# Optimization experiments

Measured on AMD Instinct MI355X. Metric: run time of the kernel, lower is better.

## Reference

```python
import jax, jax.numpy as jnp
import numpy as np

HIDDEN = 1024
D_INNER = 2048
DT_RANK = 64
STATE = 16
KCONV = 4


def setup_inputs() -> dict:
    key = jax.random.key(0)
    ks = jax.random.split(key, 9)
    s = lambda k, shape, sc=0.02: jax.random.normal(k, shape, dtype=jnp.float32) * sc
    return {
        "x": jax.random.normal(ks[0], (2, 1024, HIDDEN), dtype=jnp.float32),
        "in_proj_w": s(ks[1], (2 * D_INNER, HIDDEN)),
        "conv_w": s(ks[2], (D_INNER, 1, KCONV), 0.2),
        "conv_b": s(ks[3], (D_INNER,), 0.1),
        "x_proj_w": s(ks[4], (DT_RANK + 2 * STATE, D_INNER)),
        "dt_proj_w": s(ks[5], (D_INNER, DT_RANK), 0.1),
        "dt_proj_b": s(ks[6], (D_INNER,), 0.1),
        "A_log": s(ks[7], (D_INNER, STATE), 0.5),
        "out_proj_w": s(ks[8], (HIDDEN, D_INNER)),
    }


def _selective_scan(u, delta, A, B, C):
    # u, delta: (b,l,d); A: (d,n); B, C: (b,l,n)
    deltaA = jnp.exp(delta[..., None] * A)               # (b,l,d,n)
    dBu = (delta * u)[..., None] * B[:, :, None, :]      # (b,l,d,n)
    # scan over time axis; carry h: (b,d,n)
    deltaA_t = jnp.moveaxis(deltaA, 1, 0)                # (l,b,d,n)
    dBu_t = jnp.moveaxis(dBu, 1, 0)                      # (l,b,d,n)
    C_t = jnp.moveaxis(C, 1, 0)                          # (l,b,n)

    def step(h, inp):
        dA_i, dBu_i, C_i = inp
        h = dA_i * h + dBu_i
        y = jnp.einsum('bdn,bn->bd', h, C_i)
        return h, y

    h0 = jnp.zeros(u.shape[:1] + u.shape[2:] + (A.shape[1],), dtype=u.dtype)
    _, ys = jax.lax.scan(step, h0, (deltaA_t, dBu_t, C_t))
    return jnp.moveaxis(ys, 0, 1)                        # (b,l,d)


def reference(x, in_proj_w, conv_w, conv_b, x_proj_w, dt_proj_w, dt_proj_b, A_log, out_proj_w):
    b, l, _ = x.shape
    xr = x @ in_proj_w.T                                 # (b,l,2*d_inner)
    xs, res = jnp.split(xr, 2, axis=-1)
    # causal depthwise conv1d: pad left k-1 (matches padding=k-1 then [:l])
    xc = jnp.moveaxis(xs, 1, 2)                          # (b,d,l)
    xc = jax.lax.conv_general_dilated(
        xc, conv_w, window_strides=(1,), padding=[(KCONV - 1, 0)],
        feature_group_count=D_INNER,
        dimension_numbers=('NCH', 'OIH', 'NCH'))
    xc = xc + conv_b[None, :, None]
    xs = jnp.moveaxis(xc, 2, 1)                          # (b,l,d)
    xs = jax.nn.silu(xs)
    x_dbl = xs @ x_proj_w.T                              # (b,l,dt_rank+2n)
    dt, B, C = jnp.split(x_dbl, [DT_RANK, DT_RANK + STATE], axis=-1)
    delta = jax.nn.softplus(dt @ dt_proj_w.T + dt_proj_b)
    A = -jnp.exp(A_log.astype(jnp.float32))
    y = _selective_scan(xs, delta, A, B, C)
    y = y * jax.nn.silu(res)
    return y @ out_proj_w.T
```

## Files before the change

kernel.cpp:

```cpp
#include <hip/hip_runtime.h>

typedef unsigned short u16;
typedef __bf16 bf16x8 __attribute__((ext_vector_type(8)));
typedef float f32x4 __attribute__((ext_vector_type(4)));

__device__ inline float bf2f(u16 u) {
    unsigned int x = ((unsigned int)u) << 16;
    return __builtin_bit_cast(float, x);
}
__device__ inline u16 f2bf(float f) {
    unsigned int x = __builtin_bit_cast(unsigned int, f);
    return (u16)((x + 0x7FFFu + ((x >> 16) & 1u)) >> 16);
}
__device__ inline float sigm(float v) { return 1.f / (1.f + __expf(-v)); }
__device__ inline float ex2(float x) {
    float r; asm("v_exp_f32 %0, %1" : "=v"(r) : "v"(x)); return r;
}

__device__ __forceinline__ void gload16(const void* g, void* l) {
    __builtin_amdgcn_global_load_lds(
        (const __attribute__((address_space(1))) void*)g,
        (__attribute__((address_space(3))) void*)l, 16, 0, 0);
}

__device__ inline uint4 pack8(const float* p) {
    const float4* q = (const float4*)p;
    float4 a = q[0], b = q[1];
    union { u16 h[8]; uint4 v; } u;
    u.h[0] = f2bf(a.x); u.h[1] = f2bf(a.y); u.h[2] = f2bf(a.z); u.h[3] = f2bf(a.w);
    u.h[4] = f2bf(b.x); u.h[5] = f2bf(b.y); u.h[6] = f2bf(b.z); u.h[7] = f2bf(b.w);
    return u.v;
}

__global__ __launch_bounds__(256)
void cvt_front(const float* __restrict__ x, const float* __restrict__ inw,
               const float* __restrict__ xpw, const float* __restrict__ convw,
               const float* __restrict__ dtw,
               u16* __restrict__ x_bf, u16* __restrict__ inw_bf,
               u16* __restrict__ xpw_bf, float* __restrict__ wt,
               u16* __restrict__ dtw_bf)
{
    int bk = blockIdx.x, tid = threadIdx.x;
    if (bk < 1024) {
        int i = bk * 256 + tid;
        ((uint4*)x_bf)[i] = pack8(x + (size_t)i * 8);
    } else if (bk < 3072) {
        int i = (bk - 1024) * 256 + tid;
        ((uint4*)inw_bf)[i] = pack8(inw + (size_t)i * 8);
    } else if (bk < 3200) {
        int i = (bk - 3072) * 256 + tid;
        int row = (i * 8) >> 11;
        ((uint4*)xpw_bf)[i] = (row < 96) ? pack8(xpw + (size_t)row * 2048 + ((i * 8) & 2047))
                                         : make_uint4(0u, 0u, 0u, 0u);
    } else if (bk < 3264) {
        int i = (bk - 3200) * 256 + tid;
        ((uint4*)dtw_bf)[i] = pack8(dtw + (size_t)i * 8);
    } else {
        int i = (bk - 3264) * 256 + tid;
        wt[(i & 3) * 2048 + (i >> 2)] = convw[i];
    }
}

__global__ __launch_bounds__(256)
void cvt_bf16(const float* __restrict__ in, u16* __restrict__ out)
{
    int i = blockIdx.x * 256 + threadIdx.x;
    ((uint4*)out)[i] = pack8(in + (size_t)i * 8);
}

template<int EPI, bool OUTF32>
__global__ __launch_bounds__(256, 4)
void gemm2(const u16* __restrict__ A, int lda,
           const u16* __restrict__ B, int ldb,
           void* __restrict__ Cout, int ldc,
           int N, int ksplit, size_t zElems,
           const float* __restrict__ bias)
{
    __shared__ u16 sA[128][64];
    __shared__ u16 sB[128][64];

    const int tid  = threadIdx.x;
    const int lane = tid & 63;
    const int wave = tid >> 6;

    int nxy = gridDim.x * gridDim.y;
    int id  = blockIdx.y * gridDim.x + blockIdx.x;
    int bx, by;
    if ((nxy & 7) == 0) {
        int cpx = nxy >> 3;
        int swz = (id & 7) * cpx + (id >> 3);
        bx = swz % gridDim.x;
        by = swz / gridDim.x;
    } else { bx = blockIdx.x; by = blockIdx.y; }

    const int wm = (wave >> 1) * 64;
    const int wn = (wave & 1) * 64;
    const int m0 = by * 128;
    const int n0 = bx * 128;
    const int lm = lane & 15;
    const int g  = lane >> 4;
    const int k0 = blockIdx.z * ksplit;

    const int rr = lane >> 3;
    const int sl = lane & 7;
    const int xsl = sl ^ rr;
    const u16* gA = A + (size_t)(m0 + wave * 8 + rr) * lda + k0 + xsl * 8;
    const u16* gB = B + (size_t)(n0 + wave * 8 + rr) * ldb + k0 + xsl * 8;
    const int ldsRow = (wave * 8) * 128;

    f32x4 acc[4][4] = {};

    for (int kb = 0; kb < ksplit; kb += 64) {
        #pragma unroll
        for (int c = 0; c < 4; ++c) {
            gload16(gA + (size_t)c * 32 * lda + kb, (char*)sA + c * 4096 + ldsRow);
            gload16(gB + (size_t)c * 32 * ldb + kb, (char*)sB + c * 4096 + ldsRow);
        }
        __syncthreads();

        bf16x8 af[2][4], bfr[2][4];
        #pragma unroll
        for (int h = 0; h < 2; ++h) {
            #pragma unroll
            for (int i = 0; i < 4; ++i) {
                int ra = wm + i * 16 + lm;
                int rb = wn + i * 16 + lm;
                int chunk = (((h << 2) | g) ^ (lm & 7)) << 4;
                af[h][i]  = *(const bf16x8*)((const char*)sA + ra * 128 + chunk);
                bfr[h][i] = *(const bf16x8*)((const char*)sB + rb * 128 + chunk);
            }
        }
        #pragma unroll
        for (int h = 0; h < 2; ++h)
            #pragma unroll
            for (int i = 0; i < 4; ++i)
                #pragma unroll
                for (int j = 0; j < 4; ++j)
                    acc[i][j] = __builtin_amdgcn_mfma_f32_16x16x32_bf16(af[h][i], bfr[h][j], acc[i][j], 0, 0, 0);
        __syncthreads();
    }

    #pragma unroll
    for (int i = 0; i < 4; ++i) {
        int crow = m0 + wm + i * 16 + ((lane >> 4) << 2);
        #pragma unroll
        for (int j = 0; j < 4; ++j) {
            int ccol = n0 + wn + j * 16 + lm;
            if (ccol < N) {
                #pragma unroll
                for (int r = 0; r < 4; ++r) {
                    float v = acc[i][j][r];
                    if (EPI == 1) { v += bias[ccol]; v = (v > 20.f) ? v : log1pf(__expf(v)); }
                    if (EPI == 2 && ccol >= 2048) v *= sigm(v);
                    size_t off = (size_t)blockIdx.z * zElems + (size_t)(crow + r) * ldc + ccol;
                    if (OUTF32) ((float*)Cout)[off] = v;
                    else        ((u16*)Cout)[off]   = f2bf(v);
                }
            }
        }
    }
}

template<int EPI, bool OUTF32>
__global__ __launch_bounds__(256, 4)
void gemm_w(const u16* __restrict__ A, int lda,
            const u16* __restrict__ B, int ldb,
            void* __restrict__ Cout, int ldc,
            int N, int ksplit, size_t zElems,
            const float* __restrict__ bias)
{
    __shared__ u16 sA[64][64];
    __shared__ u16 sB[128][64];

    const int tid  = threadIdx.x;
    const int lane = tid & 63;
    const int wave = tid >> 6;

    int nxy = gridDim.x * gridDim.y;
    int id  = blockIdx.y * gridDim.x + blockIdx.x;
    int bx, by;
    if ((nxy & 7) == 0) {
        int cpx = nxy >> 3;
        int swz = (id & 7) * cpx + (id >> 3);
        bx = swz % gridDim.x;
        by = swz / gridDim.x;
    } else { bx = blockIdx.x; by = blockIdx.y; }

    const int wm = (wave >> 1) * 32;
    const int wn = (wave & 1) * 64;
    const int m0 = by * 64;
    const int n0 = bx * 128;
    const int lm = lane & 15;
    const int g  = lane >> 4;
    const int k0 = blockIdx.z * ksplit;

    const int rr = lane >> 3;
    const int sl = lane & 7;
    const int xsl = sl ^ rr;
    const u16* gA = A + (size_t)(m0 + wave * 8 + rr) * lda + k0 + xsl * 8;
    const u16* gB = B + (size_t)(n0 + wave * 8 + rr) * ldb + k0 + xsl * 8;
    const int ldsRow = (wave * 8) * 128;

    f32x4 acc[2][4] = {};

    for (int kb = 0; kb < ksplit; kb += 64) {
        #pragma unroll
        for (int c = 0; c < 2; ++c)
            gload16(gA + (size_t)c * 32 * lda + kb, (char*)sA + c * 4096 + ldsRow);
        #pragma unroll
        for (int c = 0; c < 4; ++c)
            gload16(gB + (size_t)c * 32 * ldb + kb, (char*)sB + c * 4096 + ldsRow);
        __syncthreads();

        bf16x8 af[2][2], bfr[2][4];
        #pragma unroll
        for (int h = 0; h < 2; ++h) {
            int chunk = (((h << 2) | g) ^ (lm & 7)) << 4;
            #pragma unroll
            for (int i = 0; i < 2; ++i)
                af[h][i]  = *(const bf16x8*)((const char*)sA + (wm + i * 16 + lm) * 128 + chunk);
            #pragma unroll
            for (int j = 0; j < 4; ++j)
                bfr[h][j] = *(const bf16x8*)((const char*)sB + (wn + j * 16 + lm) * 128 + chunk);
        }
        #pragma unroll
        for (int h = 0; h < 2; ++h)
            #pragma unroll
            for (int i = 0; i < 2; ++i)
                #pragma unroll
                for (int j = 0; j < 4; ++j)
                    acc[i][j] = __builtin_amdgcn_mfma_f32_16x16x32_bf16(af[h][i], bfr[h][j], acc[i][j], 0, 0, 0);
        __syncthreads();
    }

    #pragma unroll
    for (int i = 0; i < 2; ++i) {
        int crow = m0 + wm + i * 16 + ((lane >> 4) << 2);
        #pragma unroll
        for (int j = 0; j < 4; ++j) {
            int ccol = n0 + wn + j * 16 + lm;
            if (ccol < N) {
                #pragma unroll
                for (int r = 0; r < 4; ++r) {
                    float v = acc[i][j][r];
                    if (EPI == 1) { v += bias[ccol]; v = (v > 20.f) ? v : log1pf(__expf(v)); }
                    if (EPI == 2 && ccol >= 2048) v *= sigm(v);
                    size_t off = (size_t)blockIdx.z * zElems + (size_t)(crow + r) * ldc + ccol;
                    if (OUTF32) ((float*)Cout)[off] = v;
                    else        ((u16*)Cout)[off]   = f2bf(v);
                }
            }
        }
    }
}

template<int EPI, bool OUTF32>
__global__ __launch_bounds__(256, 4)
void gemm_s(const u16* __restrict__ A, int lda,
            const u16* __restrict__ B, int ldb,
            void* __restrict__ Cout, int ldc,
            int N, int ksplit, size_t zElems,
            const float* __restrict__ bias)
{
    __shared__ u16 sA[64][64];
    __shared__ u16 sB[64][64];

    const int tid  = threadIdx.x;
    const int lane = tid & 63;
    const int wave = tid >> 6;

    int nxy = gridDim.x * gridDim.y;
    int id  = blockIdx.y * gridDim.x + blockIdx.x;
    int bx, by;
    if ((nxy & 7) == 0) {
        int cpx = nxy >> 3;
        int swz = (id & 7) * cpx + (id >> 3);
        bx = swz % gridDim.x;
        by = swz / gridDim.x;
    } else { bx = blockIdx.x; by = blockIdx.y; }

    const int wm = (wave >> 1) * 32;
    const int wn = (wave & 1) * 32;
    const int m0 = by * 64;
    const int n0 = bx * 64;
    const int lm = lane & 15;
    const int g  = lane >> 4;
    const int k0 = blockIdx.z * ksplit;

    const int rr = lane >> 3;
    const int sl = lane & 7;
    const int xsl = sl ^ rr;
    const u16* gA = A + (size_t)(m0 + wave * 8 + rr) * lda + k0 + xsl * 8;
    const u16* gB = B + (size_t)(n0 + wave * 8 + rr) * ldb + k0 + xsl * 8;
    const int ldsRow = (wave * 8) * 128;

    f32x4 acc[2][2] = {};

    for (int kb = 0; kb < ksplit; kb += 64) {
        #pragma unroll
        for (int c = 0; c < 2; ++c) {
            gload16(gA + (size_t)c * 32 * lda + kb, (char*)sA + c * 4096 + ldsRow);
            gload16(gB + (size_t)c * 32 * ldb + kb, (char*)sB + c * 4096 + ldsRow);
        }
        __syncthreads();

        bf16x8 af[2][2], bfr[2][2];
        #pragma unroll
        for (int h = 0; h < 2; ++h) {
            #pragma unroll
            for (int i = 0; i < 2; ++i) {
                int ra = wm + i * 16 + lm;
                int rb = wn + i * 16 + lm;
                int chunk = (((h << 2) | g) ^ (lm & 7)) << 4;
                af[h][i]  = *(const bf16x8*)((const char*)sA + ra * 128 + chunk);
                bfr[h][i] = *(const bf16x8*)((const char*)sB + rb * 128 + chunk);
            }
        }
        #pragma unroll
        for (int h = 0; h < 2; ++h)
            #pragma unroll
            for (int i = 0; i < 2; ++i)
                #pragma unroll
                for (int j = 0; j < 2; ++j)
                    acc[i][j] = __builtin_amdgcn_mfma_f32_16x16x32_bf16(af[h][i], bfr[h][j], acc[i][j], 0, 0, 0);
        __syncthreads();
    }

    #pragma unroll
    for (int i = 0; i < 2; ++i) {
        int crow = m0 + wm + i * 16 + ((lane >> 4) << 2);
        #pragma unroll
        for (int j = 0; j < 2; ++j) {
            int ccol = n0 + wn + j * 16 + lm;
            if (ccol < N) {
                #pragma unroll
                for (int r = 0; r < 4; ++r) {
                    float v = acc[i][j][r];
                    if (EPI == 1) { v += bias[ccol]; v = (v > 20.f) ? v : log1pf(__expf(v)); }
                    size_t off = (size_t)blockIdx.z * zElems + (size_t)(crow + r) * ldc + ccol;
                    if (OUTF32) ((float*)Cout)[off] = v;
                    else        ((u16*)Cout)[off]   = f2bf(v);
                }
            }
        }
    }
}

__global__ __launch_bounds__(256)
void reduce96(const float* __restrict__ splits, u16* __restrict__ xdbl)
{
    int i = blockIdx.x * 256 + threadIdx.x;
    float acc = 0.f;
    #pragma unroll
    for (int z = 0; z < 8; ++z) acc += splits[(size_t)z * 196608 + i];
    xdbl[i] = f2bf(acc);
}

__global__ __launch_bounds__(256)
void reduce_out(const u16* __restrict__ parts, float* __restrict__ out)
{
    int i = blockIdx.x * 256 + threadIdx.x;
    float acc[8] = {};
    #pragma unroll
    for (int z = 0; z < 4; ++z) {
        uint4 v = ((const uint4*)(parts + (size_t)z * 2097152))[i];
        const u16* h = (const u16*)&v;
        #pragma unroll
        for (int e = 0; e < 8; ++e) acc[e] += bf2f(h[e]);
    }
    float4* o = (float4*)(out + (size_t)i * 8);
    o[0] = make_float4(acc[0], acc[1], acc[2], acc[3]);
    o[1] = make_float4(acc[4], acc[5], acc[6], acc[7]);
}

__global__ __launch_bounds__(256)
void conv_silu(const u16* __restrict__ xr, const float* __restrict__ wt,
               const float* __restrict__ bias, u16* __restrict__ xs)
{
    int gi = blockIdx.x * 256 + threadIdx.x;
    int d  = (gi & 255) * 8;
    int t0 = ((gi >> 8) & 255) * 4;
    int b  = gi >> 16;
    const u16* base = xr + (size_t)b * 4194304 + d;

    float bi[8], w8[4][8];
    {
        const float4* bp = (const float4*)(bias + d);
        float4 b0 = bp[0], b1 = bp[1];
        bi[0]=b0.x; bi[1]=b0.y; bi[2]=b0.z; bi[3]=b0.w;
        bi[4]=b1.x; bi[5]=b1.y; bi[6]=b1.z; bi[7]=b1.w;
        #pragma unroll
        for (int j = 0; j < 4; ++j) {
            const float4* wp = (const float4*)(wt + j * 2048 + d);
            float4 w0 = wp[0], w1 = wp[1];
            w8[j][0]=w0.x; w8[j][1]=w0.y; w8[j][2]=w0.z; w8[j][3]=w0.w;
            w8[j][4]=w1.x; w8[j][5]=w1.y; w8[j][6]=w1.z; w8[j][7]=w1.w;
        }
    }

    uint4 v[7];
    #pragma unroll
    for (int r = 0; r < 7; ++r) {
        int ti = t0 - 3 + r;
        v[r] = (ti >= 0) ? *(const uint4*)(base + (size_t)ti * 4096)
                         : make_uint4(0u, 0u, 0u, 0u);
    }

    #pragma unroll
    for (int tt = 0; tt < 4; ++tt) {
        float acc[8];
        #pragma unroll
        for (int e = 0; e < 8; ++e) acc[e] = bi[e];
        #pragma unroll
        for (int j = 0; j < 4; ++j) {
            const u16* h = (const u16*)&v[tt + j];
            #pragma unroll
            for (int e = 0; e < 8; ++e) acc[e] = fmaf(w8[j][e], bf2f(h[e]), acc[e]);
        }
        union { u16 h[8]; uint4 u; } o;
        #pragma unroll
        for (int e = 0; e < 8; ++e) { float x = acc[e]; o.h[e] = f2bf(x * sigm(x)); }
        *(uint4*)(xs + (size_t)b * 2097152 + (size_t)(t0 + tt) * 2048 + d) = o.u;
    }
}

template<int PHC>
__global__ __launch_bounds__(256)
void scan_chunk(const u16* __restrict__ deltag, u16* __restrict__ xsg,
                const u16* __restrict__ xdbl, const float* __restrict__ A_log,
                const u16* __restrict__ xr, float* __restrict__ summ,
                float* __restrict__ ssum)
{
    const int tid = threadIdx.x;
    const int d0 = blockIdx.x * 256;
    const int c  = blockIdx.y;
    const int b  = blockIdx.z;
    const int d  = d0 + tid;
    const int tok0 = b * 1024 + c * 32;

    __shared__ u16 s_del[32][256];
    __shared__ u16 s_uu[32][256];
    __shared__ u16 s_bc[32][32];
    __shared__ u16 s_res[PHC ? 32 : 1][PHC ? 256 : 1];
    __shared__ u16 s_y[PHC ? 32 : 1][PHC ? 256 : 1];

    for (int i = tid; i < 1024; i += 256) {
        int tl = i >> 5, v = i & 31;
        size_t tok = (size_t)(tok0 + tl);
        *(uint4*)&s_del[tl][v * 8] = *(const uint4*)&deltag[tok * 4096 + d0 + v * 8];
        *(uint4*)&s_uu[tl][v * 8]  = *(const uint4*)&xsg[tok * 2048 + d0 + v * 8];
        if (PHC)
            *(uint4*)&s_res[tl][v * 8] = *(const uint4*)&xr[tok * 4096 + 2048 + d0 + v * 8];
    }
    for (int i = tid; i < 1024; i += 256) {
        int tl = i >> 5, j = i & 31;
        s_bc[tl][j] = xdbl[(size_t)(tok0 + tl) * 96 + 64 + j];
    }

    float Ar[16], h[16];
    {
        const float4* Ap = (const float4*)(A_log + (size_t)d * 16);
        #pragma unroll
        for (int q = 0; q < 4; ++q) {
            float4 a = Ap[q];
            Ar[q * 4 + 0] = -__expf(a.x) * 1.44269504f;
            Ar[q * 4 + 1] = -__expf(a.y) * 1.44269504f;
            Ar[q * 4 + 2] = -__expf(a.z) * 1.44269504f;
            Ar[q * 4 + 3] = -__expf(a.w) * 1.44269504f;
        }
    }
    if (PHC) {
        const float4* hp = (const float4*)&summ[((size_t)(b * 32 + c) * 2048 + d) * 16];
        #pragma unroll
        for (int q = 0; q < 4; ++q) {
            float4 v = hp[q];
            h[q * 4 + 0] = v.x; h[q * 4 + 1] = v.y; h[q * 4 + 2] = v.z; h[q * 4 + 3] = v.w;
        }
    } else {
        #pragma unroll
        for (int n = 0; n < 16; ++n) h[n] = 0.f;
    }
    __syncthreads();

    float S = 0.f;
    #pragma unroll 4
    for (int tl = 0; tl < 32; ++tl) {
        float dlt = bf2f(s_del[tl][tid]);
        float du = dlt * bf2f(s_uu[tl][tid]);
        if (!PHC) S += dlt;
        #pragma unroll
        for (int n = 0; n < 16; ++n)
            h[n] = fmaf(ex2(dlt * Ar[n]), h[n], du * bf2f(s_bc[tl][n]));
        if (PHC) {
            float y = 0.f;
            #pragma unroll
            for (int n = 0; n < 16; ++n)
                y = fmaf(h[n], bf2f(s_bc[tl][16 + n]), y);
            s_y[tl][tid] = f2bf(y * bf2f(s_res[tl][tid]));
        }
    }

    if (!PHC) {
        float4* bp = (float4*)&summ[((size_t)(b * 32 + c) * 2048 + d) * 16];
        #pragma unroll
        for (int q = 0; q < 4; ++q)
            bp[q] = make_float4(h[q * 4], h[q * 4 + 1], h[q * 4 + 2], h[q * 4 + 3]);
        ssum[(size_t)(b * 32 + c) * 2048 + d] = S;
    } else {
        __syncthreads();
        for (int i = tid; i < 1024; i += 256) {
            int tl = i >> 5, v = i & 31;
            *(uint4*)&xsg[(size_t)(tok0 + tl) * 2048 + d0 + v * 8] = *(uint4*)&s_y[tl][v * 8];
        }
    }
}

__global__ __launch_bounds__(256)
void scan_phaseB(float* __restrict__ summ, const float* __restrict__ ssum,
                 const float* __restrict__ A_log)
{
    int g = blockIdx.x * 256 + threadIdx.x;
    int n = g & 15;
    int d = (g >> 4) & 2047;
    int b = g >> 15;
    float An2 = -__expf(A_log[(size_t)d * 16 + n]) * 1.44269504f;
    size_t base = ((size_t)(b * 32) * 2048 + d) * 16 + n;
    float bc[32], Sc[32];
    #pragma unroll
    for (int c = 0; c < 32; ++c) bc[c] = summ[base + (size_t)c * 32768];
    #pragma unroll
    for (int c = 0; c < 32; ++c) Sc[c] = ssum[(size_t)(b * 32 + c) * 2048 + d];
    float h = 0.f;
    #pragma unroll
    for (int c = 0; c < 32; ++c) {
        float nb = bc[c];
        bc[c] = h;
        h = fmaf(ex2(An2 * Sc[c]), h, nb);
    }
    #pragma unroll
    for (int c = 0; c < 32; ++c) summ[base + (size_t)c * 32768] = bc[c];
}

__global__ void sentinel_kernel(float* out, float v) { out[0] = v; }

extern "C" void kernel_launch(void* const* d_in, const int* in_sizes, int n_in,
                              void* d_out, int out_size, void* d_ws, size_t ws_size,
                              hipStream_t stream)
{
    const float* x         = (const float*)d_in[0];
    const float* in_w      = (const float*)d_in[1];
    const float* conv_w    = (const float*)d_in[2];
    const float* conv_b    = (const float*)d_in[3];
    const float* xproj_w   = (const float*)d_in[4];
    const float* dtproj_w  = (const float*)d_in[5];
    const float* dtproj_b  = (const float*)d_in[6];
    const float* A_log     = (const float*)d_in[7];
    const float* outproj_w = (const float*)d_in[8];
    float* out = (float*)d_out;

    static const int EXP[9] = {2097152, 4194304, 8192, 2048, 196608, 131072, 2048, 32768, 2097152};
    int bad = -1;
    if (n_in != 9) bad = 9;
    else { for (int i = 0; i < 9; ++i) if (in_sizes[i] != EXP[i]) { bad = i; break; } }
    if (bad < 0 && out_size != 2097152) bad = 10;
    if (bad < 0 && ws_size < 34734080u) bad = 11;
    if (bad >= 0) {
        sentinel_kernel<<<1, 1, 0, stream>>>(out, 131072.f * (1.f + (float)bad / 16.f));
        return;
    }

    char* ws = (char*)d_ws;
    u16*   xr      = (u16*)(ws);
    u16*   xs      = (u16*)(ws + 16777216);
    u16*   xdbl    = (u16*)(ws + 25165824);
    char*  R       = ws + 25559040;
    u16*   x_bf    = xs;
    u16*   inw_bf  = (u16*)(R);
    u16*   xpw_bf  = (u16*)(R + 8388608);
    float* wt      = (float*)(R + 8912896);
    u16*   dtw_bf  = (u16*)out;
    float* splits  = (float*)(R);
    float* summ    = (float*)(R);
    float* ssum    = (float*)(R + 8388608);
    u16*   opw_bf  = (u16*)(R);
    u16*   oparts  = xr;

    cvt_front<<<3296, 256, 0, stream>>>(x, in_w, xproj_w, conv_w, dtproj_w,
                                        x_bf, inw_bf, xpw_bf, wt, dtw_bf);
    gemm_w<2, false><<<dim3(32, 32, 1), 256, 0, stream>>>(
        x_bf, 1024, inw_bf, 1024, xr, 4096, 4096, 1024, 0, nullptr);
    conv_silu<<<512, 256, 0, stream>>>(xr, wt, conv_b, xs);
    gemm_s<0, true><<<dim3(2, 32, 8), 256, 0, stream>>>(
        xs, 2048, xpw_bf, 2048, splits, 96, 96, 256, 196608, nullptr);
    reduce96<<<768, 256, 0, stream>>>(splits, xdbl);
    gemm_s<1, false><<<dim3(32, 32, 1), 256, 0, stream>>>(
        xdbl, 96, dtw_bf, 64, xr, 4096, 2048, 64, 0, dtproj_b);
    scan_chunk<0><<<dim3(8, 32, 2), 256, 0, stream>>>(xr, xs, xdbl, A_log, xr, summ, ssum);
    scan_phaseB<<<256, 256, 0, stream>>>(summ, ssum, A_log);
    scan_chunk<1><<<dim3(8, 32, 2), 256, 0, stream>>>(xr, xs, xdbl, A_log, xr, summ, ssum);
    cvt_bf16<<<1024, 256, 0, stream>>>(outproj_w, opw_bf);
    gemm2<0, false><<<dim3(8, 16, 4), 256, 0, stream>>>(
        xs, 2048, opw_bf, 2048, oparts, 1024, 1024, 512, 2097152, nullptr);
    reduce_out<<<1024, 256, 0, stream>>>(oparts, out);
}
```

Measured before the change: 219.8 us.

## Double-buffer in_proj GEMM, fold out_proj weight conversion into front, vectorize reduce96

```diff
diff --git a/kernel.cpp b/kernel.cpp
--- a/kernel.cpp
+++ b/kernel.cpp
@@ -35,10 +35,10 @@
 __global__ __launch_bounds__(256)
 void cvt_front(const float* __restrict__ x, const float* __restrict__ inw,
                const float* __restrict__ xpw, const float* __restrict__ convw,
-               const float* __restrict__ dtw,
+               const float* __restrict__ dtw, const float* __restrict__ opw,
                u16* __restrict__ x_bf, u16* __restrict__ inw_bf,
                u16* __restrict__ xpw_bf, float* __restrict__ wt,
-               u16* __restrict__ dtw_bf)
+               u16* __restrict__ dtw_bf, u16* __restrict__ opw_bf)
 {
     int bk = blockIdx.x, tid = threadIdx.x;
     if (bk < 1024) {
@@ -55,17 +55,13 @@
     } else if (bk < 3264) {
         int i = (bk - 3200) * 256 + tid;
         ((uint4*)dtw_bf)[i] = pack8(dtw + (size_t)i * 8);
+    } else if (bk < 4288) {
+        int i = (bk - 3264) * 256 + tid;
+        ((uint4*)opw_bf)[i] = pack8(opw + (size_t)i * 8);
     } else {
-        int i = (bk - 3264) * 256 + tid;
+        int i = (bk - 4288) * 256 + tid;
         wt[(i & 3) * 2048 + (i >> 2)] = convw[i];
     }
-}
-
-__global__ __launch_bounds__(256)
-void cvt_bf16(const float* __restrict__ in, u16* __restrict__ out)
-{
-    int i = blockIdx.x * 256 + threadIdx.x;
-    ((uint4*)out)[i] = pack8(in + (size_t)i * 8);
 }
 
 template<int EPI, bool OUTF32>
@@ -162,15 +158,15 @@
 }
 
 template<int EPI, bool OUTF32>
-__global__ __launch_bounds__(256, 4)
+__global__ __launch_bounds__(256, 3)
 void gemm_w(const u16* __restrict__ A, int lda,
             const u16* __restrict__ B, int ldb,
             void* __restrict__ Cout, int ldc,
             int N, int ksplit, size_t zElems,
             const float* __restrict__ bias)
 {
-    __shared__ u16 sA[64][64];
-    __shared__ u16 sB[128][64];
+    __shared__ u16 sA[2][64][64];
+    __shared__ u16 sB[2][128][64];
 
     const int tid  = threadIdx.x;
     const int lane = tid & 63;
@@ -203,25 +199,39 @@
 
     f32x4 acc[2][4] = {};
 
+    {
+        #pragma unroll
+        for (int c = 0; c < 2; ++c)
+            gload16(gA + (size_t)c * 32 * lda, (char*)sA[0] + c * 4096 + ldsRow);
+        #pragma unroll
+        for (int c = 0; c < 4; ++c)
+            gload16(gB + (size_t)c * 32 * ldb, (char*)sB[0] + c * 4096 + ldsRow);
+    }
+
+    int cur = 0;
     for (int kb = 0; kb < ksplit; kb += 64) {
-        #pragma unroll
-        for (int c = 0; c < 2; ++c)
-            gload16(gA + (size_t)c * 32 * lda + kb, (char*)sA + c * 4096 + ldsRow);
-        #pragma unroll
-        for (int c = 0; c < 4; ++c)
-            gload16(gB + (size_t)c * 32 * ldb + kb, (char*)sB + c * 4096 + ldsRow);
         __syncthreads();
-
+        if (kb + 64 < ksplit) {
+            #pragma unroll
+            for (int c = 0; c < 2; ++c)
+                gload16(gA + (size_t)c * 32 * lda + kb + 64, (char*)sA[cur ^ 1] + c * 4096 + ldsRow);
+            #pragma unroll
+            for (int c = 0; c < 4; ++c)
+                gload16(gB + (size_t)c * 32 * ldb + kb + 64, (char*)sB[cur ^ 1] + c * 4096 + ldsRow);
+        }
+
+        const char* bA = (const char*)sA[cur];
+        const char* bB = (const char*)sB[cur];
         bf16x8 af[2][2], bfr[2][4];
         #pragma unroll
         for (int h = 0; h < 2; ++h) {
             int chunk = (((h << 2) | g) ^ (lm & 7)) << 4;
             #pragma unroll
             for (int i = 0; i < 2; ++i)
-                af[h][i]  = *(const bf16x8*)((const char*)sA + (wm + i * 16 + lm) * 128 + chunk);
+                af[h][i]  = *(const bf16x8*)(bA + (wm + i * 16 + lm) * 128 + chunk);
             #pragma unroll
             for (int j = 0; j < 4; ++j)
-                bfr[h][j] = *(const bf16x8*)((const char*)sB + (wn + j * 16 + lm) * 128 + chunk);
+                bfr[h][j] = *(const bf16x8*)(bB + (wn + j * 16 + lm) * 128 + chunk);
         }
         #pragma unroll
         for (int h = 0; h < 2; ++h)
@@ -230,7 +240,7 @@
                 #pragma unroll
                 for (int j = 0; j < 4; ++j)
                     acc[i][j] = __builtin_amdgcn_mfma_f32_16x16x32_bf16(af[h][i], bfr[h][j], acc[i][j], 0, 0, 0);
-        __syncthreads();
+        cur ^= 1;
     }
 
     #pragma unroll
@@ -350,10 +360,18 @@
 void reduce96(const float* __restrict__ splits, u16* __restrict__ xdbl)
 {
     int i = blockIdx.x * 256 + threadIdx.x;
-    float acc = 0.f;
-    #pragma unroll
-    for (int z = 0; z < 8; ++z) acc += splits[(size_t)z * 196608 + i];
-    xdbl[i] = f2bf(acc);
+    float acc[8] = {};
+    #pragma unroll
+    for (int z = 0; z < 8; ++z) {
+        const float4* p = (const float4*)(splits + (size_t)z * 196608 + (size_t)i * 8);
+        float4 a = p[0], b = p[1];
+        acc[0] += a.x; acc[1] += a.y; acc[2] += a.z; acc[3] += a.w;
+        acc[4] += b.x; acc[5] += b.y; acc[6] += b.z; acc[7] += b.w;
+    }
+    union { u16 h[8]; uint4 v; } o;
+    #pragma unroll
+    for (int e = 0; e < 8; ++e) o.h[e] = f2bf(acc[e]);
+    ((uint4*)xdbl)[i] = o.v;
 }
 
 __global__ __launch_bounds__(256)
@@ -579,26 +597,25 @@
     u16*   xpw_bf  = (u16*)(R + 8388608);
     float* wt      = (float*)(R + 8912896);
     u16*   dtw_bf  = (u16*)out;
+    u16*   opw_bf  = (u16*)((char*)out + 262144);
     float* splits  = (float*)(R);
     float* summ    = (float*)(R);
     float* ssum    = (float*)(R + 8388608);
-    u16*   opw_bf  = (u16*)(R);
     u16*   oparts  = xr;
 
-    cvt_front<<<3296, 256, 0, stream>>>(x, in_w, xproj_w, conv_w, dtproj_w,
-                                        x_bf, inw_bf, xpw_bf, wt, dtw_bf);
+    cvt_front<<<4320, 256, 0, stream>>>(x, in_w, xproj_w, conv_w, dtproj_w, outproj_w,
+                                        x_bf, inw_bf, xpw_bf, wt, dtw_bf, opw_bf);
     gemm_w<2, false><<<dim3(32, 32, 1), 256, 0, stream>>>(
         x_bf, 1024, inw_bf, 1024, xr, 4096, 4096, 1024, 0, nullptr);
     conv_silu<<<512, 256, 0, stream>>>(xr, wt, conv_b, xs);
     gemm_s<0, true><<<dim3(2, 32, 8), 256, 0, stream>>>(
         xs, 2048, xpw_bf, 2048, splits, 96, 96, 256, 196608, nullptr);
-    reduce96<<<768, 256, 0, stream>>>(splits, xdbl);
+    reduce96<<<96, 256, 0, stream>>>(splits, xdbl);
     gemm_s<1, false><<<dim3(32, 32, 1), 256, 0, stream>>>(
         xdbl, 96, dtw_bf, 64, xr, 4096, 2048, 64, 0, dtproj_b);
     scan_chunk<0><<<dim3(8, 32, 2), 256, 0, stream>>>(xr, xs, xdbl, A_log, xr, summ, ssum);
     scan_phaseB<<<256, 256, 0, stream>>>(summ, ssum, A_log);
     scan_chunk<1><<<dim3(8, 32, 2), 256, 0, stream>>>(xr, xs, xdbl, A_log, xr, summ, ssum);
-    cvt_bf16<<<1024, 256, 0, stream>>>(outproj_w, opw_bf);
     gemm2<0, false><<<dim3(8, 16, 4), 256, 0, stream>>>(
         xs, 2048, opw_bf, 2048, oparts, 1024, 1024, 512, 2097152, nullptr);
     reduce_out<<<1024, 256, 0, stream>>>(oparts, out);
```

Result: slower. 227.6 us (+3.6%).
